# Optimization experiments

Hardware: AMD Instinct MI355X
Metric: run time of the kernel (lower is better)

The kernel has to match this reference:

```python
import jax, jax.numpy as jnp
import numpy as np

NPM = 100          # neurons per module
NMOD = 3
NN = NPM * NMOD    # 300 neurons
NF = 20            # input features
OUT = 50
T = 500
B = 1024

def retanh(x):
    # ReTanh: tanh(x) for x>0 else 0  == max(tanh(x), 0)
    return jnp.maximum(jnp.tanh(x), 0.0)

def setup_inputs() -> dict:
    key = jax.random.key(0)
    ks = jax.random.split(key, 8)
    data = jax.random.normal(ks[0], (T, NF + 1, B), dtype=jnp.float32)
    # J: block-structured recurrent weights (dense within modules, sparse between);
    # forward math only uses the dense matrix, so random dense init scaled ~1/sqrt(npm)
    J = jax.random.normal(ks[1], (NN, NN), dtype=jnp.float32) * (1.2 / np.sqrt(NPM))
    I = jax.random.normal(ks[2], (NN, NF), dtype=jnp.float32) * (1.0 / np.sqrt(NF))
    I = I.at[-NPM:, :].set(0.0)  # last module receives no image input
    S = jax.random.normal(ks[3], (NN, 1), dtype=jnp.float32)
    Bb = jax.random.uniform(ks[4], (NN, 1), dtype=jnp.float32, minval=-1.0, maxval=1.0)
    x0 = jax.random.normal(ks[5], (NN,), dtype=jnp.float32)
    fc_w = jax.random.normal(ks[6], (OUT, NPM), dtype=jnp.float32) * (1.0 / np.sqrt(NPM))
    fc_b = jax.random.normal(ks[7], (OUT,), dtype=jnp.float32) * 0.01
    return {"data": data, "J": J, "I": I, "S": S, "Bb": Bb, "x0": x0,
            "fc_w": fc_w, "fc_b": fc_b}

def reference(data, J, I, S, Bb, x0, fc_w, fc_b):
    nf = I.shape[1]
    bsz = data.shape[2]
    npm = fc_w.shape[1]
    x_init = jnp.tile(x0, (bsz, 1))          # [B, NN]
    r_init = retanh(x_init)                  # prev_output at first step

    def step(carry, d):
        x, r = carry                          # x: [B,NN], r: [B,NN]
        image = d[:nf]                        # [NF, B]
        hold = d[nf:]                         # [1, B]
        recur = r @ J.T                       # [B, NN]
        inp = image.T @ I.T + hold.T * S.T    # [B, NN]
        tdx = -x + recur + inp + Bb.T
        pre = x + tdx / 10.0                  # Euler step, dt/tau = 1/10
        out = retanh(pre)
        y = out[:, :npm] @ fc_w.T + fc_b      # [B, OUT]
        return (pre, out), y

    _, ys = jax.lax.scan(step, (x_init, r_init), data)
    return ys  # [T, B, OUT]
```

## Files before the change

kernel.cpp:

```cpp
#include <hip/hip_runtime.h>
#include <math.h>

#define NNEUR 300
#define NFEAT 20
#define NPAD  320
#define MAUGP 336
#define NOUT  50
#define NPMAC 100
#define TSTEPS 500
#define BATCH 1024
#define NWAVE 16
#define MCHUNK 21
#define RROWS 17
#define LROWS 4
#define NJ 5

__global__ void build_w_kernel(const float* __restrict__ J,
                               const float* __restrict__ I,
                               const float* __restrict__ S,
                               const float* __restrict__ Bb,
                               float* __restrict__ W) {
    int e = blockIdx.x * 256 + threadIdx.x;
    if (e >= MAUGP * NPAD) return;
    int m = e / NPAD, n = e % NPAD;
    float v = 0.0f;
    if (n < NNEUR) {
        if (m < NNEUR)                   v = J[n * NNEUR + m];
        else if (m < NNEUR + NFEAT)      v = I[n * NFEAT + (m - NNEUR)];
        else if (m == NNEUR + NFEAT)     v = S[n];
        else if (m == NNEUR + NFEAT + 1) v = Bb[n];
    }
    W[e] = v;
}

__global__ __launch_bounds__(1024, 4) void rnn_kernel(
    const float* __restrict__ W,
    const float* __restrict__ data,
    const float* __restrict__ x0,
    const float* __restrict__ fcw,
    const float* __restrict__ fcb,
    float* __restrict__ out)
{
    __shared__ __align__(16) float Wl[NWAVE][LROWS][NPAD];
    __shared__ __align__(16) float part[8][4][NPAD];
    __shared__ __align__(16) float raug[MAUGP][4];
    __shared__ __align__(16) float xs[4][NPAD];
    __shared__ float fcwt[NPMAC][NOUT];
    __shared__ float fcbs[NOUT];

    const int tid = threadIdx.x;
    const int wid = tid >> 6;
    const int l   = tid & 63;
    const int b0  = blockIdx.x * 4;
    const int m0  = wid * MCHUNK;

    for (int i = tid; i < MAUGP * 4; i += 1024) ((float*)raug)[i] = 0.0f;
    for (int i = tid; i < NPMAC * NOUT; i += 1024) {
        int p = i / NOUT, o = i - p * NOUT;
        fcwt[p][o] = fcw[o * NPMAC + p];
    }
    if (tid < NOUT) fcbs[tid] = fcb[tid];
    __syncthreads();

    for (int i = tid; i < NNEUR; i += 1024) {
        float xv = x0[i];
        float rv = fmaxf(tanhf(xv), 0.0f);
        #pragma unroll
        for (int b = 0; b < 4; ++b) { xs[b][i] = xv; raug[i][b] = rv; }
    }
    if (tid < 4) raug[NNEUR + NFEAT + 1][tid] = 1.0f;

    float wr[RROWS * NJ];
    #pragma unroll
    for (int i = 0; i < RROWS; ++i)
        #pragma unroll
        for (int j = 0; j < NJ; ++j)
            wr[i * NJ + j] = W[(size_t)(m0 + i) * NPAD + 64 * j + l];
    #pragma unroll
    for (int i = 0; i < LROWS; ++i)
        #pragma unroll
        for (int j = 0; j < NJ; ++j)
            Wl[wid][i][64 * j + l] = W[(size_t)(m0 + RROWS + i) * NPAD + 64 * j + l];

    float4 dstage = make_float4(0.f, 0.f, 0.f, 0.f);
    if (tid < NFEAT + 1)
        dstage = *reinterpret_cast<const float4*>(data + (size_t)tid * BATCH + b0);
    __syncthreads();

    for (int t = 0; t < TSTEPS; ++t) {
        if (tid < NFEAT + 1) {
            *reinterpret_cast<float4*>(&raug[NNEUR + tid][0]) = dstage;
            if (t + 1 < TSTEPS)
                dstage = *reinterpret_cast<const float4*>(
                    data + ((size_t)(t + 1) * (NFEAT + 1) + tid) * BATCH + b0);
        }
        __syncthreads();

        float acc[NJ * 4];
        #pragma unroll
        for (int k = 0; k < NJ * 4; ++k) acc[k] = 0.0f;

        #pragma unroll
        for (int i = 0; i < RROWS; ++i) {
            const float4 rv = *reinterpret_cast<const float4*>(&raug[m0 + i][0]);
            const float rb[4] = {rv.x, rv.y, rv.z, rv.w};
            #pragma unroll
            for (int j = 0; j < NJ; ++j)
                #pragma unroll
                for (int b = 0; b < 4; ++b)
                    acc[j * 4 + b] += wr[i * NJ + j] * rb[b];
        }
        #pragma unroll
        for (int i = 0; i < LROWS; ++i) {
            const float4 rv = *reinterpret_cast<const float4*>(&raug[m0 + RROWS + i][0]);
            const float rb[4] = {rv.x, rv.y, rv.z, rv.w};
            float wv[NJ];
            #pragma unroll
            for (int j = 0; j < NJ; ++j) wv[j] = Wl[wid][i][64 * j + l];
            #pragma unroll
            for (int j = 0; j < NJ; ++j)
                #pragma unroll
                for (int b = 0; b < 4; ++b)
                    acc[j * 4 + b] += wv[j] * rb[b];
        }

        if (wid < 8) {
            #pragma unroll
            for (int j = 0; j < NJ; ++j)
                #pragma unroll
                for (int b = 0; b < 4; ++b)
                    part[wid][b][64 * j + l] = acc[j * 4 + b];
        }
        __syncthreads();
        if (wid >= 8) {
            #pragma unroll
            for (int j = 0; j < NJ; ++j)
                #pragma unroll
                for (int b = 0; b < 4; ++b)
                    part[wid - 8][b][64 * j + l] += acc[j * 4 + b];
        }
        __syncthreads();

        {
            int b = tid / NPAD;
            int n = tid - b * NPAD;
            if (n < NNEUR) {
                float s = 0.0f;
                #pragma unroll
                for (int w8 = 0; w8 < 8; ++w8) s += part[w8][b][n];
                float xo  = xs[b][n];
                float pre = xo + (s - xo) * 0.1f;
                xs[b][n] = pre;
                raug[n][b] = fmaxf(tanhf(pre), 0.0f);
            }
            if (tid < 256) {
                int n2 = 64 + tid;
                if (n2 < NNEUR) {
                    float s = 0.0f;
                    #pragma unroll
                    for (int w8 = 0; w8 < 8; ++w8) s += part[w8][3][n2];
                    float xo  = xs[3][n2];
                    float pre = xo + (s - xo) * 0.1f;
                    xs[3][n2] = pre;
                    raug[n2][3] = fmaxf(tanhf(pre), 0.0f);
                }
            }
        }
        __syncthreads();

        if (tid < 4 * NOUT) {
            int b = tid / NOUT, o = tid - b * NOUT;
            float y = fcbs[o];
            #pragma unroll 4
            for (int p = 0; p < NPMAC; ++p)
                y += raug[p][b] * fcwt[p][o];
            out[((size_t)t * BATCH + b0 + b) * NOUT + o] = y;
        }
    }
}

extern "C" void kernel_launch(void* const* d_in, const int* in_sizes, int n_in,
                              void* d_out, int out_size, void* d_ws, size_t ws_size,
                              hipStream_t stream) {
    const float* data = (const float*)d_in[0];
    const float* J    = (const float*)d_in[1];
    const float* I    = (const float*)d_in[2];
    const float* S    = (const float*)d_in[3];
    const float* Bb   = (const float*)d_in[4];
    const float* x0   = (const float*)d_in[5];
    const float* fcw  = (const float*)d_in[6];
    const float* fcb  = (const float*)d_in[7];
    float* out = (float*)d_out;
    float* W   = (float*)d_ws;

    int wtot = MAUGP * NPAD;
    build_w_kernel<<<(wtot + 255) / 256, 256, 0, stream>>>(J, I, S, Bb, W);
    rnn_kernel<<<256, 1024, 0, stream>>>(W, data, x0, fcw, fcb, out);
}
```

Baseline: 2.767 ms.

## Vectorize weight and partial-sum accesses with float4 and split FC output reduction

Changes the per-lane column mapping from strided (64*j + l) to contiguous 4*l plus a 256+l tail, so register weights, LDS weights and partial sums load and store as float4. It adds empty asm barriers to pin the weight registers. The FC output stage now splits each 100-term dot product across 4 lanes and combines them with shuffles, using 800 threads instead of 200, which shortens that serial per-timestep tail. The aim is fewer LDS instructions and less latency per step, at the risk of bank conflicts from the float4 stride pattern and of register pressure.

After: 9.919 ms. 258% more time.

```diff
diff --git a/kernel.cpp b/kernel.cpp
--- a/kernel.cpp
+++ b/kernel.cpp
@@ -13,7 +13,6 @@
 #define MCHUNK 21
 #define RROWS 17
 #define LROWS 4
-#define NJ 5
 
 __global__ void build_w_kernel(const float* __restrict__ J,
                                const float* __restrict__ I,
@@ -70,17 +69,24 @@
     }
     if (tid < 4) raug[NNEUR + NFEAT + 1][tid] = 1.0f;
 
-    float wr[RROWS * NJ];
+    float4 w4[RROWS];
+    float  wt[RROWS];
     #pragma unroll
-    for (int i = 0; i < RROWS; ++i)
-        #pragma unroll
-        for (int j = 0; j < NJ; ++j)
-            wr[i * NJ + j] = W[(size_t)(m0 + i) * NPAD + 64 * j + l];
+    for (int i = 0; i < RROWS; ++i) {
+        w4[i] = *reinterpret_cast<const float4*>(&W[(size_t)(m0 + i) * NPAD + 4 * l]);
+        wt[i] = W[(size_t)(m0 + i) * NPAD + 256 + l];
+    }
     #pragma unroll
-    for (int i = 0; i < LROWS; ++i)
-        #pragma unroll
-        for (int j = 0; j < NJ; ++j)
-            Wl[wid][i][64 * j + l] = W[(size_t)(m0 + RROWS + i) * NPAD + 64 * j + l];
+    for (int i = 0; i < RROWS; ++i) {
+        asm volatile("" : "+v"(w4[i].x), "+v"(w4[i].y), "+v"(w4[i].z), "+v"(w4[i].w));
+        asm volatile("" : "+v"(wt[i]));
+    }
+    #pragma unroll
+    for (int i = 0; i < LROWS; ++i) {
+        *reinterpret_cast<float4*>(&Wl[wid][i][4 * l]) =
+            *reinterpret_cast<const float4*>(&W[(size_t)(m0 + RROWS + i) * NPAD + 4 * l]);
+        Wl[wid][i][256 + l] = W[(size_t)(m0 + RROWS + i) * NPAD + 256 + l];
+    }
 
     float4 dstage = make_float4(0.f, 0.f, 0.f, 0.f);
     if (tid < NFEAT + 1)
@@ -96,48 +102,62 @@
         }
         __syncthreads();
 
-        float acc[NJ * 4];
-        #pragma unroll
-        for (int k = 0; k < NJ * 4; ++k) acc[k] = 0.0f;
+        float acc[4][4];
+        float acct[4];
+        #pragma unroll
+        for (int j = 0; j < 4; ++j)
+            #pragma unroll
+            for (int b = 0; b < 4; ++b) acc[j][b] = 0.0f;
+        #pragma unroll
+        for (int b = 0; b < 4; ++b) acct[b] = 0.0f;
 
         #pragma unroll
         for (int i = 0; i < RROWS; ++i) {
             const float4 rv = *reinterpret_cast<const float4*>(&raug[m0 + i][0]);
             const float rb[4] = {rv.x, rv.y, rv.z, rv.w};
-            #pragma unroll
-            for (int j = 0; j < NJ; ++j)
+            const float wj[4] = {w4[i].x, w4[i].y, w4[i].z, w4[i].w};
+            #pragma unroll
+            for (int j = 0; j < 4; ++j)
                 #pragma unroll
                 for (int b = 0; b < 4; ++b)
-                    acc[j * 4 + b] += wr[i * NJ + j] * rb[b];
+                    acc[j][b] += wj[j] * rb[b];
+            #pragma unroll
+            for (int b = 0; b < 4; ++b) acct[b] += wt[i] * rb[b];
         }
         #pragma unroll
         for (int i = 0; i < LROWS; ++i) {
             const float4 rv = *reinterpret_cast<const float4*>(&raug[m0 + RROWS + i][0]);
             const float rb[4] = {rv.x, rv.y, rv.z, rv.w};
-            float wv[NJ];
-            #pragma unroll
-            for (int j = 0; j < NJ; ++j) wv[j] = Wl[wid][i][64 * j + l];
-            #pragma unroll
-            for (int j = 0; j < NJ; ++j)
+            const float4 wv = *reinterpret_cast<const float4*>(&Wl[wid][i][4 * l]);
+            const float wlt = Wl[wid][i][256 + l];
+            const float wj[4] = {wv.x, wv.y, wv.z, wv.w};
+            #pragma unroll
+            for (int j = 0; j < 4; ++j)
                 #pragma unroll
                 for (int b = 0; b < 4; ++b)
-                    acc[j * 4 + b] += wv[j] * rb[b];
+                    acc[j][b] += wj[j] * rb[b];
+            #pragma unroll
+            for (int b = 0; b < 4; ++b) acct[b] += wlt * rb[b];
         }
 
         if (wid < 8) {
             #pragma unroll
-            for (int j = 0; j < NJ; ++j)
-                #pragma unroll
-                for (int b = 0; b < 4; ++b)
-                    part[wid][b][64 * j + l] = acc[j * 4 + b];
+            for (int b = 0; b < 4; ++b) {
+                float4 v = make_float4(acc[0][b], acc[1][b], acc[2][b], acc[3][b]);
+                *reinterpret_cast<float4*>(&part[wid][b][4 * l]) = v;
+                part[wid][b][256 + l] = acct[b];
+            }
         }
         __syncthreads();
         if (wid >= 8) {
             #pragma unroll
-            for (int j = 0; j < NJ; ++j)
-                #pragma unroll
-                for (int b = 0; b < 4; ++b)
-                    part[wid - 8][b][64 * j + l] += acc[j * 4 + b];
+            for (int b = 0; b < 4; ++b) {
+                float4 p4 = *reinterpret_cast<float4*>(&part[wid - 8][b][4 * l]);
+                p4.x += acc[0][b]; p4.y += acc[1][b];
+                p4.z += acc[2][b]; p4.w += acc[3][b];
+                *reinterpret_cast<float4*>(&part[wid - 8][b][4 * l]) = p4;
+                part[wid - 8][b][256 + l] += acct[b];
+            }
         }
         __syncthreads();
 
@@ -168,13 +188,18 @@
         }
         __syncthreads();
 
-        if (tid < 4 * NOUT) {
-            int b = tid / NOUT, o = tid - b * NOUT;
-            float y = fcbs[o];
-            #pragma unroll 4
-            for (int p = 0; p < NPMAC; ++p)
-                y += raug[p][b] * fcwt[p][o];
-            out[((size_t)t * BATCH + b0 + b) * NOUT + o] = y;
+        if (tid < 800) {
+            int pair = tid >> 2, seg = tid & 3;
+            int b = pair / NOUT, o = pair - (pair / NOUT) * NOUT;
+            int pb = seg * 25;
+            float y = 0.0f;
+            #pragma unroll 5
+            for (int k = 0; k < 25; ++k)
+                y += raug[pb + k][b] * fcwt[pb + k][o];
+            y += __shfl_down(y, 1, 4);
+            y += __shfl_down(y, 2, 4);
+            if (seg == 0)
+                out[((size_t)t * BATCH + b0 + b) * NOUT + o] = y + fcbs[o];
         }
     }
 }
```

## Process eight batch columns per block with packed FMA and streamed weights

Applied to the files above, without the earlier changes.

Each block now handles 8 batch columns instead of 4, so 128 blocks are launched instead of 256. The weight matrix is no longer kept in registers and LDS; it is re-read from global memory (L2) every timestep as float4 loads, and the math uses packed two-wide float vectors. Recurrent state is stored as float pairs, and the readout dot product is split across two lanes joined with a shuffle. This halves the grid to raise weight reuse per batch column and cut LDS footprint. In exchange each timestep pays repeated global weight loads on the serial critical path, and fewer blocks may leave compute units idle.

After: 4.549 ms. 1.64x slower.

```diff
diff --git a/kernel.cpp b/kernel.cpp
--- a/kernel.cpp
+++ b/kernel.cpp
@@ -4,16 +4,17 @@
 #define NNEUR 300
 #define NFEAT 20
 #define NPAD  320
-#define MAUGP 336
+#define MDIM  336
 #define NOUT  50
 #define NPMAC 100
 #define TSTEPS 500
 #define BATCH 1024
 #define NWAVE 16
 #define MCHUNK 21
-#define RROWS 17
-#define LROWS 4
-#define NJ 5
+#define NBCOL 8
+#define PSTR  328
+
+typedef float v2f __attribute__((ext_vector_type(2)));
 
 __global__ void build_w_kernel(const float* __restrict__ J,
                                const float* __restrict__ I,
@@ -21,7 +22,7 @@
                                const float* __restrict__ Bb,
                                float* __restrict__ W) {
     int e = blockIdx.x * 256 + threadIdx.x;
-    if (e >= MAUGP * NPAD) return;
+    if (e >= MDIM * NPAD) return;
     int m = e / NPAD, n = e % NPAD;
     float v = 0.0f;
     if (n < NNEUR) {
@@ -41,140 +42,142 @@
     const float* __restrict__ fcb,
     float* __restrict__ out)
 {
-    __shared__ __align__(16) float Wl[NWAVE][LROWS][NPAD];
-    __shared__ __align__(16) float part[8][4][NPAD];
-    __shared__ __align__(16) float raug[MAUGP][4];
-    __shared__ __align__(16) float xs[4][NPAD];
+    __shared__ __align__(16) float part[8][NBCOL][PSTR];
+    __shared__ __align__(16) v2f   raugP[4][MDIM];
+    __shared__ __align__(16) float xs[NBCOL][NPAD];
     __shared__ float fcwt[NPMAC][NOUT];
     __shared__ float fcbs[NOUT];
 
     const int tid = threadIdx.x;
     const int wid = tid >> 6;
     const int l   = tid & 63;
-    const int b0  = blockIdx.x * 4;
+    const int b0  = blockIdx.x * NBCOL;
     const int m0  = wid * MCHUNK;
 
-    for (int i = tid; i < MAUGP * 4; i += 1024) ((float*)raug)[i] = 0.0f;
+    for (int i = tid; i < 4 * MDIM; i += 1024) ((v2f*)raugP)[i] = (v2f)0.0f;
     for (int i = tid; i < NPMAC * NOUT; i += 1024) {
-        int p = i / NOUT, o = i - p * NOUT;
+        int p = i / NOUT, o = i - (i / NOUT) * NOUT;
         fcwt[p][o] = fcw[o * NPMAC + p];
     }
     if (tid < NOUT) fcbs[tid] = fcb[tid];
     __syncthreads();
-
     for (int i = tid; i < NNEUR; i += 1024) {
         float xv = x0[i];
         float rv = fmaxf(tanhf(xv), 0.0f);
         #pragma unroll
-        for (int b = 0; b < 4; ++b) { xs[b][i] = xv; raug[i][b] = rv; }
-    }
-    if (tid < 4) raug[NNEUR + NFEAT + 1][tid] = 1.0f;
-
-    float wr[RROWS * NJ];
-    #pragma unroll
-    for (int i = 0; i < RROWS; ++i)
-        #pragma unroll
-        for (int j = 0; j < NJ; ++j)
-            wr[i * NJ + j] = W[(size_t)(m0 + i) * NPAD + 64 * j + l];
-    #pragma unroll
-    for (int i = 0; i < LROWS; ++i)
-        #pragma unroll
-        for (int j = 0; j < NJ; ++j)
-            Wl[wid][i][64 * j + l] = W[(size_t)(m0 + RROWS + i) * NPAD + 64 * j + l];
-
-    float4 dstage = make_float4(0.f, 0.f, 0.f, 0.f);
-    if (tid < NFEAT + 1)
-        dstage = *reinterpret_cast<const float4*>(data + (size_t)tid * BATCH + b0);
+        for (int b = 0; b < NBCOL; ++b) xs[b][i] = xv;
+        v2f rr; rr.x = rv; rr.y = rv;
+        #pragma unroll
+        for (int bp = 0; bp < 4; ++bp) raugP[bp][i] = rr;
+    }
+    if (tid < 168) {
+        int f = tid >> 3, bc = tid & 7;
+        float d0 = data[(size_t)f * BATCH + b0 + bc];
+        reinterpret_cast<float*>(&raugP[bc >> 1][NNEUR + f])[bc & 1] = d0;
+    }
+    if (tid < 8)
+        reinterpret_cast<float*>(&raugP[tid >> 1][NNEUR + NFEAT + 1])[tid & 1] = 1.0f;
     __syncthreads();
 
+    const int df = tid >> 3, dbc = tid & 7;
+    float dpre = 0.0f;
+
     for (int t = 0; t < TSTEPS; ++t) {
-        if (tid < NFEAT + 1) {
-            *reinterpret_cast<float4*>(&raug[NNEUR + tid][0]) = dstage;
-            if (t + 1 < TSTEPS)
-                dstage = *reinterpret_cast<const float4*>(
-                    data + ((size_t)(t + 1) * (NFEAT + 1) + tid) * BATCH + b0);
-        }
-        __syncthreads();
-
-        float acc[NJ * 4];
-        #pragma unroll
-        for (int k = 0; k < NJ * 4; ++k) acc[k] = 0.0f;
-
-        #pragma unroll
-        for (int i = 0; i < RROWS; ++i) {
-            const float4 rv = *reinterpret_cast<const float4*>(&raug[m0 + i][0]);
-            const float rb[4] = {rv.x, rv.y, rv.z, rv.w};
-            #pragma unroll
-            for (int j = 0; j < NJ; ++j)
-                #pragma unroll
-                for (int b = 0; b < 4; ++b)
-                    acc[j * 4 + b] += wr[i * NJ + j] * rb[b];
-        }
-        #pragma unroll
-        for (int i = 0; i < LROWS; ++i) {
-            const float4 rv = *reinterpret_cast<const float4*>(&raug[m0 + RROWS + i][0]);
-            const float rb[4] = {rv.x, rv.y, rv.z, rv.w};
-            float wv[NJ];
-            #pragma unroll
-            for (int j = 0; j < NJ; ++j) wv[j] = Wl[wid][i][64 * j + l];
-            #pragma unroll
-            for (int j = 0; j < NJ; ++j)
-                #pragma unroll
-                for (int b = 0; b < 4; ++b)
-                    acc[j * 4 + b] += wv[j] * rb[b];
+        if (tid < 168 && t + 1 < TSTEPS)
+            dpre = data[((size_t)(t + 1) * (NFEAT + 1) + df) * BATCH + b0 + dbc];
+
+        v2f acc01[NBCOL], acc23[NBCOL], accT[4];
+        #pragma unroll
+        for (int b = 0; b < NBCOL; ++b) { acc01[b] = (v2f)0.0f; acc23[b] = (v2f)0.0f; }
+        #pragma unroll
+        for (int bp = 0; bp < 4; ++bp) accT[bp] = (v2f)0.0f;
+
+        const float* Wp = W + (size_t)m0 * NPAD;
+        #pragma unroll 7
+        for (int i = 0; i < MCHUNK; ++i) {
+            const float4 w4 = *reinterpret_cast<const float4*>(Wp + (size_t)i * NPAD + 4 * l);
+            const float  wt = Wp[(size_t)i * NPAD + 256 + l];
+            v2f w01; w01.x = w4.x; w01.y = w4.y;
+            v2f w23; w23.x = w4.z; w23.y = w4.w;
+            v2f wtt; wtt.x = wt;   wtt.y = wt;
+            const int row = m0 + i;
+            #pragma unroll
+            for (int bp = 0; bp < 4; ++bp) {
+                const v2f rp = raugP[bp][row];
+                v2f rs0; rs0.x = rp.x; rs0.y = rp.x;
+                v2f rs1; rs1.x = rp.y; rs1.y = rp.y;
+                acc01[2 * bp]     += w01 * rs0;
+                acc23[2 * bp]     += w23 * rs0;
+                acc01[2 * bp + 1] += w01 * rs1;
+                acc23[2 * bp + 1] += w23 * rs1;
+                accT[bp]          += wtt * rp;
+            }
         }
 
         if (wid < 8) {
             #pragma unroll
-            for (int j = 0; j < NJ; ++j)
-                #pragma unroll
-                for (int b = 0; b < 4; ++b)
-                    part[wid][b][64 * j + l] = acc[j * 4 + b];
+            for (int b = 0; b < NBCOL; ++b) {
+                float4 v; v.x = acc01[b].x; v.y = acc01[b].y;
+                          v.z = acc23[b].x; v.w = acc23[b].y;
+                *reinterpret_cast<float4*>(&part[wid][b][4 * l]) = v;
+            }
+            #pragma unroll
+            for (int bp = 0; bp < 4; ++bp) {
+                part[wid][2 * bp][256 + l]     = accT[bp].x;
+                part[wid][2 * bp + 1][256 + l] = accT[bp].y;
+            }
         }
         __syncthreads();
         if (wid >= 8) {
-            #pragma unroll
-            for (int j = 0; j < NJ; ++j)
-                #pragma unroll
-                for (int b = 0; b < 4; ++b)
-                    part[wid - 8][b][64 * j + l] += acc[j * 4 + b];
+            const int w8 = wid - 8;
+            #pragma unroll
+            for (int b = 0; b < NBCOL; ++b) {
+                float4 p4 = *reinterpret_cast<float4*>(&part[w8][b][4 * l]);
+                p4.x += acc01[b].x; p4.y += acc01[b].y;
+                p4.z += acc23[b].x; p4.w += acc23[b].y;
+                *reinterpret_cast<float4*>(&part[w8][b][4 * l]) = p4;
+            }
+            #pragma unroll
+            for (int bp = 0; bp < 4; ++bp) {
+                part[w8][2 * bp][256 + l]     += accT[bp].x;
+                part[w8][2 * bp + 1][256 + l] += accT[bp].y;
+            }
         }
         __syncthreads();
 
-        {
-            int b = tid / NPAD;
-            int n = tid - b * NPAD;
-            if (n < NNEUR) {
-                float s = 0.0f;
-                #pragma unroll
-                for (int w8 = 0; w8 < 8; ++w8) s += part[w8][b][n];
-                float xo  = xs[b][n];
-                float pre = xo + (s - xo) * 0.1f;
-                xs[b][n] = pre;
-                raug[n][b] = fmaxf(tanhf(pre), 0.0f);
-            }
-            if (tid < 256) {
-                int n2 = 64 + tid;
-                if (n2 < NNEUR) {
-                    float s = 0.0f;
-                    #pragma unroll
-                    for (int w8 = 0; w8 < 8; ++w8) s += part[w8][3][n2];
-                    float xo  = xs[3][n2];
+        #pragma unroll
+        for (int pass = 0; pass < 3; ++pass) {
+            int item = tid + pass * 1024;
+            if (item < NBCOL * NPAD) {
+                int b = item / NPAD, n = item - NPAD * b;
+                if (n < NNEUR) {
+                    float s = part[0][b][n] + part[1][b][n] + part[2][b][n] + part[3][b][n]
+                            + part[4][b][n] + part[5][b][n] + part[6][b][n] + part[7][b][n];
+                    float xo  = xs[b][n];
                     float pre = xo + (s - xo) * 0.1f;
-                    xs[3][n2] = pre;
-                    raug[n2][3] = fmaxf(tanhf(pre), 0.0f);
+                    xs[b][n] = pre;
+                    reinterpret_cast<float*>(&raugP[b >> 1][n])[b & 1] =
+                        fmaxf(tanhf(pre), 0.0f);
                 }
             }
         }
+        if (tid < 168 && t + 1 < TSTEPS)
+            reinterpret_cast<float*>(&raugP[dbc >> 1][NNEUR + df])[dbc & 1] = dpre;
         __syncthreads();
 
-        if (tid < 4 * NOUT) {
-            int b = tid / NOUT, o = tid - b * NOUT;
-            float y = fcbs[o];
-            #pragma unroll 4
-            for (int p = 0; p < NPMAC; ++p)
-                y += raug[p][b] * fcwt[p][o];
-            out[((size_t)t * BATCH + b0 + b) * NOUT + o] = y;
+        if (tid < 800) {
+            int pair = tid >> 1, seg = tid & 1;
+            int bD = pair / NOUT, oD = pair - (pair / NOUT) * NOUT;
+            int pb = seg * 50;
+            float y = 0.0f;
+            #pragma unroll 10
+            for (int k = 0; k < 50; ++k) {
+                float rr = reinterpret_cast<const float*>(&raugP[bD >> 1][pb + k])[bD & 1];
+                y += rr * fcwt[pb + k][oD];
+            }
+            y += __shfl_down(y, 1, 2);
+            if (seg == 0)
+                out[((size_t)t * BATCH + b0 + bD) * NOUT + oD] = y + fcbs[oD];
         }
     }
 }
@@ -193,7 +196,7 @@
     float* out = (float*)d_out;
     float* W   = (float*)d_ws;
 
-    int wtot = MAUGP * NPAD;
+    int wtot = MDIM * NPAD;
     build_w_kernel<<<(wtot + 255) / 256, 256, 0, stream>>>(J, I, S, Bb, W);
-    rnn_kernel<<<256, 1024, 0, stream>>>(W, data, x0, fcw, fcb, out);
+    rnn_kernel<<<BATCH / NBCOL, 1024, 0, stream>>>(W, data, x0, fcw, fcb, out);
 }
```
